# Optimization experiments

Hardware: AMD Instinct MI355X
Metric: run time of the kernel (lower is better)

Reference implementation:

```python
import jax, jax.numpy as jnp
import numpy as np
from jax import lax

D_MODEL = 1024
D_INNER = 2048   # expand=2.0
D_CONV = 4
D_STATE = 16     # delta=16
DT_RANK = 64     # ceil(d_model/16)
B, L = 4, 2048


def setup_inputs() -> dict:
    key = jax.random.key(0)
    ks = jax.random.split(key, 8)
    x = jax.random.normal(ks[0], (B, L, D_MODEL), jnp.float32)
    W_in = jax.random.normal(ks[1], (2 * D_INNER, D_MODEL), jnp.float32) * 0.02
    conv_w = jax.random.normal(ks[2], (D_INNER, D_CONV), jnp.float32) * 0.2
    conv_b = jnp.zeros((D_INNER,), jnp.float32)
    W_x = jax.random.normal(ks[3], (DT_RANK + 2 * D_STATE, D_INNER), jnp.float32) * 0.02
    W_dt = jax.random.normal(ks[4], (D_INNER, DT_RANK), jnp.float32) * 0.1
    # bias so softplus(b_dt) ~ dt in [1e-3, 1e-1] as in mamba_ssm init
    b_dt = jax.random.normal(ks[5], (D_INNER,), jnp.float32) * 0.3 - 4.0
    # mamba S4D-real init: A = -(1..d_state)
    A_log = jnp.log(jnp.tile(jnp.arange(1, D_STATE + 1, dtype=jnp.float32), (D_INNER, 1)))
    D_skip = jnp.ones((D_INNER,), jnp.float32)
    W_out = jax.random.normal(ks[6], (D_MODEL, D_INNER), jnp.float32) * 0.02
    return {"x": x, "W_in": W_in, "conv_w": conv_w, "conv_b": conv_b,
            "W_x": W_x, "W_dt": W_dt, "b_dt": b_dt, "A_log": A_log,
            "D_skip": D_skip, "W_out": W_out}


def reference(x, W_in, conv_w, conv_b, W_x, W_dt, b_dt, A_log, D_skip, W_out):
    Bsz, Lseq, _ = x.shape
    # input projection -> (B, L, 2*d_inner); split into ssm branch xi and gate z
    xz = jnp.einsum('bld,ed->ble', x, W_in)
    xi, z = jnp.split(xz, 2, axis=-1)
    # causal depthwise conv over sequence (pad left by d_conv-1), then SiLU
    xc = lax.conv_general_dilated(
        xi.transpose(0, 2, 1),               # (B, d_inner, L)
        conv_w[:, None, :],                  # (d_inner, 1, d_conv)
        window_strides=(1,),
        padding=[(D_CONV - 1, 0)],
        dimension_numbers=('NCH', 'OIH', 'NCH'),
        feature_group_count=D_INNER)
    xc = jax.nn.silu(xc + conv_b[None, :, None]).transpose(0, 2, 1)  # (B, L, d_inner)
    # data-dependent SSM params
    xdbl = jnp.einsum('bld,ed->ble', xc, W_x)          # (B, L, dt_rank + 2*d_state)
    dt_lo = xdbl[..., :DT_RANK]
    Bm = xdbl[..., DT_RANK:DT_RANK + D_STATE]          # (B, L, d_state)
    Cm = xdbl[..., DT_RANK + D_STATE:]                 # (B, L, d_state)
    dt = jax.nn.softplus(jnp.einsum('blr,dr->bld', dt_lo, W_dt) + b_dt)  # (B, L, d_inner)
    A = -jnp.exp(A_log)                                # (d_inner, d_state)

    def step(h, inp):
        dt_t, x_t, B_t, C_t = inp                      # (B,Di), (B,Di), (B,S), (B,S)
        dA = jnp.exp(dt_t[..., None] * A)              # (B, Di, S)
        h = dA * h + (dt_t * x_t)[..., None] * B_t[:, None, :]
        y = jnp.einsum('bds,bs->bd', h, C_t)
        return h, y

    h0 = jnp.zeros((Bsz, D_INNER, D_STATE), x.dtype)
    inputs = (dt.transpose(1, 0, 2), xc.transpose(1, 0, 2),
              Bm.transpose(1, 0, 2), Cm.transpose(1, 0, 2))
    _, ys = lax.scan(step, h0, inputs)                 # ys: (L, B, d_inner)
    y = ys.transpose(1, 0, 2) + xc * D_skip            # skip connection
    y = y * jax.nn.silu(z)                             # gating
    return jnp.einsum('bld,ed->ble', y, W_out)         # (B, L, d_model)
```

## Files before the change

kernel.cpp:

```cpp
#include <hip/hip_runtime.h>
#include <hip/hip_bf16.h>

#define DM    1024
#define DI    2048
#define DCONV 4
#define DSTATE 16
#define DRANK 64
#define BB    4
#define LSEQ  2048
#define MM    (BB*LSEQ)
#define CHUNK 64

typedef _Float16 f16x8 __attribute__((ext_vector_type(8)));
typedef _Float16 f16x4 __attribute__((ext_vector_type(4)));
typedef float    f32x4 __attribute__((ext_vector_type(4)));

#define SWIZ(row, g) ((((row) * 4) + ((g) ^ ((row) & 3) ^ (((row) >> 2) & 1))) * 8)

__global__ __launch_bounds__(256) void split_kernel(
    const float* __restrict__ in, _Float16* __restrict__ hi,
    _Float16* __restrict__ lo, int n4)
{
    const int i = blockIdx.x * 256 + threadIdx.x;
    if (i >= n4) return;
    const float4 v = ((const float4*)in)[i];
    _Float16 h[4], l[4];
    h[0] = (_Float16)v.x; l[0] = (_Float16)(v.x - (float)h[0]);
    h[1] = (_Float16)v.y; l[1] = (_Float16)(v.y - (float)h[1]);
    h[2] = (_Float16)v.z; l[2] = (_Float16)(v.z - (float)h[2]);
    h[3] = (_Float16)v.w; l[3] = (_Float16)(v.w - (float)h[3]);
    *(uint2*)&hi[(size_t)i * 4] = *(uint2*)h;
    *(uint2*)&lo[(size_t)i * 4] = *(uint2*)l;
}

__global__ __launch_bounds__(256) void gemm_nt_split(
    float* __restrict__ C,
    const _Float16* __restrict__ Ah, const _Float16* __restrict__ Al,
    const _Float16* __restrict__ Bh, const _Float16* __restrict__ Bl,
    int M, int N, int K)
{
    __shared__ __align__(16) _Float16 sAh[128 * 32];
    __shared__ __align__(16) _Float16 sAl[128 * 32];
    __shared__ __align__(16) _Float16 sBh[128 * 32];
    __shared__ __align__(16) _Float16 sBl[128 * 32];

    const int t = threadIdx.x;
    const int m0 = blockIdx.y * 128, n0 = blockIdx.x * 128;
    const int l = t & 63, w = t >> 6;
    const int wr = w >> 1, wc = w & 1;
    const int fr = l & 15, fg = l >> 4;

    f32x4 acc[4][4];
    const f32x4 zz = {0.f, 0.f, 0.f, 0.f};
#pragma unroll
    for (int i = 0; i < 4; ++i)
#pragma unroll
        for (int j = 0; j < 4; ++j) acc[i][j] = zz;

    const int r0 = t >> 2, c0 = t & 3;
    const int r1 = r0 + 64, c1 = c0;
    const int d0 = SWIZ(r0, c0), d1 = SWIZ(r1, c1);
    const size_t gA0 = (size_t)(m0 + r0) * K + c0 * 8;
    const size_t gA1 = (size_t)(m0 + r1) * K + c1 * 8;
    const size_t gB0 = (size_t)(n0 + r0) * K + c0 * 8;
    const size_t gB1 = (size_t)(n0 + r1) * K + c1 * 8;

    uint4 vAh0 = *(const uint4*)&Ah[gA0], vAh1 = *(const uint4*)&Ah[gA1];
    uint4 vAl0 = *(const uint4*)&Al[gA0], vAl1 = *(const uint4*)&Al[gA1];
    uint4 vBh0 = *(const uint4*)&Bh[gB0], vBh1 = *(const uint4*)&Bh[gB1];
    uint4 vBl0 = *(const uint4*)&Bl[gB0], vBl1 = *(const uint4*)&Bl[gB1];

    const int nk = K / 32;
    for (int kt = 0; kt < nk; ++kt) {
        __syncthreads();
        *(uint4*)&sAh[d0] = vAh0;  *(uint4*)&sAh[d1] = vAh1;
        *(uint4*)&sAl[d0] = vAl0;  *(uint4*)&sAl[d1] = vAl1;
        *(uint4*)&sBh[d0] = vBh0;  *(uint4*)&sBh[d1] = vBh1;
        *(uint4*)&sBl[d0] = vBl0;  *(uint4*)&sBl[d1] = vBl1;
        __syncthreads();

        if (kt + 1 < nk) {
            const size_t o = (size_t)(kt + 1) * 32;
            vAh0 = *(const uint4*)&Ah[gA0 + o]; vAh1 = *(const uint4*)&Ah[gA1 + o];
            vAl0 = *(const uint4*)&Al[gA0 + o]; vAl1 = *(const uint4*)&Al[gA1 + o];
            vBh0 = *(const uint4*)&Bh[gB0 + o]; vBh1 = *(const uint4*)&Bh[gB1 + o];
            vBl0 = *(const uint4*)&Bl[gB0 + o]; vBl1 = *(const uint4*)&Bl[gB1 + o];
        }

        f16x8 fbh[4], fbl[4];
#pragma unroll
        for (int nr = 0; nr < 4; ++nr) {
            const int row = wc * 64 + nr * 16 + fr;
            const int ad = SWIZ(row, fg);
            fbh[nr] = *(const f16x8*)&sBh[ad];
            fbl[nr] = *(const f16x8*)&sBl[ad];
        }
#pragma unroll
        for (int mr = 0; mr < 4; ++mr) {
            const int row = wr * 64 + mr * 16 + fr;
            const int ad = SWIZ(row, fg);
            const f16x8 fah = *(const f16x8*)&sAh[ad];
            const f16x8 fal = *(const f16x8*)&sAl[ad];
#pragma unroll
            for (int nr = 0; nr < 4; ++nr) {
                acc[mr][nr] = __builtin_amdgcn_mfma_f32_16x16x32_f16(
                    fah, fbh[nr], acc[mr][nr], 0, 0, 0);
                acc[mr][nr] = __builtin_amdgcn_mfma_f32_16x16x32_f16(
                    fah, fbl[nr], acc[mr][nr], 0, 0, 0);
                acc[mr][nr] = __builtin_amdgcn_mfma_f32_16x16x32_f16(
                    fal, fbh[nr], acc[mr][nr], 0, 0, 0);
            }
        }
    }

#pragma unroll
    for (int mr = 0; mr < 4; ++mr)
#pragma unroll
        for (int nr = 0; nr < 4; ++nr) {
            const int col = n0 + wc * 64 + nr * 16 + fr;
#pragma unroll
            for (int q = 0; q < 4; ++q) {
                const int rowc = m0 + wr * 64 + mr * 16 + fg * 4 + q;
                C[(size_t)rowc * N + col] = acc[mr][nr][q];
            }
        }
}

__global__ __launch_bounds__(256) void conv_silu_split_kernel(
    const float* __restrict__ xi, const float* __restrict__ cw,
    const float* __restrict__ cb, _Float16* __restrict__ xch,
    _Float16* __restrict__ xcl)
{
    const int idx = blockIdx.x * 256 + threadIdx.x;
    const int d4 = idx & (DI / 4 - 1);
    const int bl = idx / (DI / 4);
    const int l  = bl & (LSEQ - 1);
    const int d  = d4 * 4;

    float4 acc = *(const float4*)&cb[d];
    const float4 w0 = *(const float4*)&cw[(d + 0) * 4];
    const float4 w1 = *(const float4*)&cw[(d + 1) * 4];
    const float4 w2 = *(const float4*)&cw[(d + 2) * 4];
    const float4 w3 = *(const float4*)&cw[(d + 3) * 4];

#pragma unroll
    for (int k = 0; k < 4; ++k) {
        const int ll = l - 3 + k;
        if (ll < 0) continue;
        const float4 xv = *(const float4*)&xi[(size_t)(bl - 3 + k) * DI + d];
        const float wk0 = (k == 0) ? w0.x : (k == 1) ? w0.y : (k == 2) ? w0.z : w0.w;
        const float wk1 = (k == 0) ? w1.x : (k == 1) ? w1.y : (k == 2) ? w1.z : w1.w;
        const float wk2 = (k == 0) ? w2.x : (k == 1) ? w2.y : (k == 2) ? w2.z : w2.w;
        const float wk3 = (k == 0) ? w3.x : (k == 1) ? w3.y : (k == 2) ? w3.z : w3.w;
        acc.x = fmaf(xv.x, wk0, acc.x);
        acc.y = fmaf(xv.y, wk1, acc.y);
        acc.z = fmaf(xv.z, wk2, acc.z);
        acc.w = fmaf(xv.w, wk3, acc.w);
    }
    acc.x = acc.x / (1.f + __expf(-acc.x));
    acc.y = acc.y / (1.f + __expf(-acc.y));
    acc.z = acc.z / (1.f + __expf(-acc.z));
    acc.w = acc.w / (1.f + __expf(-acc.w));

    _Float16 h[4], lo4[4];
    h[0] = (_Float16)acc.x; lo4[0] = (_Float16)(acc.x - (float)h[0]);
    h[1] = (_Float16)acc.y; lo4[1] = (_Float16)(acc.y - (float)h[1]);
    h[2] = (_Float16)acc.z; lo4[2] = (_Float16)(acc.z - (float)h[2]);
    h[3] = (_Float16)acc.w; lo4[3] = (_Float16)(acc.w - (float)h[3]);
    *(uint2*)&xch[(size_t)bl * DI + d] = *(uint2*)h;
    *(uint2*)&xcl[(size_t)bl * DI + d] = *(uint2*)lo4;
}

__global__ __launch_bounds__(256) void xdbl_mfma_kernel(
    const _Float16* __restrict__ Xh, const _Float16* __restrict__ Xl,
    const _Float16* __restrict__ Wh, const _Float16* __restrict__ Wl,
    float* __restrict__ xdbl)
{
    __shared__ __align__(16) _Float16 sXh[64 * 32];
    __shared__ __align__(16) _Float16 sXl[64 * 32];
    __shared__ __align__(16) _Float16 sWh[96 * 32];
    __shared__ __align__(16) _Float16 sWl[96 * 32];

    const int t = threadIdx.x;
    const int m0 = blockIdx.x * 64;
    const int l = t & 63, w = t >> 6;
    const int fr = l & 15, fg = l >> 4;

    f32x4 acc[6];
    const f32x4 zz = {0.f, 0.f, 0.f, 0.f};
#pragma unroll
    for (int i = 0; i < 6; ++i) acc[i] = zz;

    const int ar = t >> 2, ac = t & 3;
    const int da = SWIZ(ar, ac);
    const size_t gX = (size_t)(m0 + ar) * DI + ac * 8;
    const int br0 = t >> 2, bc0 = t & 3;
    const int db0 = SWIZ(br0, bc0);
    const size_t gW0 = (size_t)br0 * DI + bc0 * 8;
    const bool has1 = t < 128;
    const int br1 = (t + 256) >> 2, bc1 = t & 3;
    const int db1 = SWIZ(br1, bc1);
    const size_t gW1 = (size_t)br1 * DI + bc1 * 8;

    uint4 vXh = *(const uint4*)&Xh[gX], vXl = *(const uint4*)&Xl[gX];
    uint4 vWh0 = *(const uint4*)&Wh[gW0], vWl0 = *(const uint4*)&Wl[gW0];
    uint4 vWh1, vWl1;
    if (has1) { vWh1 = *(const uint4*)&Wh[gW1]; vWl1 = *(const uint4*)&Wl[gW1]; }

    const int nk = DI / 32;
    for (int kt = 0; kt < nk; ++kt) {
        __syncthreads();
        *(uint4*)&sXh[da] = vXh;   *(uint4*)&sXl[da] = vXl;
        *(uint4*)&sWh[db0] = vWh0; *(uint4*)&sWl[db0] = vWl0;
        if (has1) { *(uint4*)&sWh[db1] = vWh1; *(uint4*)&sWl[db1] = vWl1; }
        __syncthreads();

        if (kt + 1 < nk) {
            const size_t o = (size_t)(kt + 1) * 32;
            vXh = *(const uint4*)&Xh[gX + o];   vXl = *(const uint4*)&Xl[gX + o];
            vWh0 = *(const uint4*)&Wh[gW0 + o]; vWl0 = *(const uint4*)&Wl[gW0 + o];
            if (has1) { vWh1 = *(const uint4*)&Wh[gW1 + o]; vWl1 = *(const uint4*)&Wl[gW1 + o]; }
        }

        const int aad = SWIZ(w * 16 + fr, fg);
        const f16x8 fah = *(const f16x8*)&sXh[aad];
        const f16x8 fal = *(const f16x8*)&sXl[aad];
#pragma unroll
        for (int nr = 0; nr < 6; ++nr) {
            const int bad = SWIZ(nr * 16 + fr, fg);
            const f16x8 fbh = *(const f16x8*)&sWh[bad];
            const f16x8 fbl = *(const f16x8*)&sWl[bad];
            acc[nr] = __builtin_amdgcn_mfma_f32_16x16x32_f16(fah, fbh, acc[nr], 0, 0, 0);
            acc[nr] = __builtin_amdgcn_mfma_f32_16x16x32_f16(fah, fbl, acc[nr], 0, 0, 0);
            acc[nr] = __builtin_amdgcn_mfma_f32_16x16x32_f16(fal, fbh, acc[nr], 0, 0, 0);
        }
    }

#pragma unroll
    for (int nr = 0; nr < 6; ++nr) {
        const int col = nr * 16 + fr;
#pragma unroll
        for (int q = 0; q < 4; ++q) {
            const int row = m0 + w * 16 + fg * 4 + q;
            xdbl[(size_t)row * 96 + col] = acc[nr][q];
        }
    }
}

__global__ __launch_bounds__(256) void dt_kernel(
    const float* __restrict__ xdbl, const float* __restrict__ Wdt,
    const float* __restrict__ bdt, float* __restrict__ dt)
{
    __shared__ float s[16][64];
    const int t = threadIdx.x;
    const int m0 = blockIdx.y * 16;

    {
        const int row = t >> 4, c4 = t & 15;
        *(float4*)&s[row][c4 * 4] =
            *(const float4*)&xdbl[(size_t)(m0 + row) * 96 + c4 * 4];
    }
    __syncthreads();

    const int n = blockIdx.x * 256 + t;
    float4 w[16];
#pragma unroll
    for (int k4 = 0; k4 < 16; ++k4)
        w[k4] = *(const float4*)&Wdt[(size_t)n * 64 + k4 * 4];
    const float bd = bdt[n];

#pragma unroll
    for (int i = 0; i < 16; ++i) {
        float acc = bd;
#pragma unroll
        for (int k4 = 0; k4 < 16; ++k4) {
            acc += s[i][k4*4+0] * w[k4].x + s[i][k4*4+1] * w[k4].y
                 + s[i][k4*4+2] * w[k4].z + s[i][k4*4+3] * w[k4].w;
        }
        const float sp = (acc > 20.f) ? acc : log1pf(__expf(acc));
        dt[(size_t)(m0 + i) * DI + n] = sp;
    }
}

__global__ __launch_bounds__(256) void scan_kernel(
    const float* __restrict__ dt,
    const _Float16* __restrict__ xch, const _Float16* __restrict__ xcl,
    const float* __restrict__ xdbl, const float* z,
    const float* __restrict__ A_log, const float* __restrict__ D_skip,
    float* y)
{
    __shared__ float s_dt[CHUNK][16];
    __shared__ float s_xc[CHUNK][16];
    __shared__ float s_z [CHUNK][16];
    __shared__ float s_B [CHUNK][16];
    __shared__ float s_C [CHUNK][16];
    __shared__ float s_p [16][16][17];
    __shared__ float s_D [16];

    const int t = threadIdx.x;
    const int g = t >> 4;
    const int s = t & 15;
    const int c = blockIdx.x * 16 + g;
    const int b = c >> 11;
    const int d = c & (DI - 1);
    const int d0 = (blockIdx.x * 16) & (DI - 1);

    const int lr = t >> 2;
    const int lc = t & 3;

    if (t < 16) s_D[t] = D_skip[d0 + t];

    const float Acoef = -__expf(A_log[d * DSTATE + s]);
    const size_t rbase = (size_t)b * LSEQ;

    float h = 0.f;
    float4 r_dt, r_z, r_B, r_C;
    f16x4 r_xh, r_xl;

    {
        const size_t row = rbase + lr;
        r_dt = *(const float4*)&dt[row * DI + d0 + lc * 4];
        r_xh = *(const f16x4*)&xch[row * DI + d0 + lc * 4];
        r_xl = *(const f16x4*)&xcl[row * DI + d0 + lc * 4];
        r_z  = *(const float4*)&z [row * DI + d0 + lc * 4];
        r_B  = *(const float4*)&xdbl[row * 96 + DRANK + lc * 4];
        r_C  = *(const float4*)&xdbl[row * 96 + DRANK + DSTATE + lc * 4];
    }

    for (int ch = 0; ch < LSEQ / CHUNK; ++ch) {
        __syncthreads();
        *(float4*)&s_dt[lr][lc * 4] = r_dt;
        {
            float4 xf;
            xf.x = (float)r_xh[0] + (float)r_xl[0];
            xf.y = (float)r_xh[1] + (float)r_xl[1];
            xf.z = (float)r_xh[2] + (float)r_xl[2];
            xf.w = (float)r_xh[3] + (float)r_xl[3];
            *(float4*)&s_xc[lr][lc * 4] = xf;
        }
        *(float4*)&s_z [lr][lc * 4] = r_z;
        *(float4*)&s_B [lr][lc * 4] = r_B;
        *(float4*)&s_C [lr][lc * 4] = r_C;
        __syncthreads();

        if (ch + 1 < LSEQ / CHUNK) {
            const size_t row = rbase + (size_t)(ch + 1) * CHUNK + lr;
            r_dt = *(const float4*)&dt[row * DI + d0 + lc * 4];
            r_xh = *(const f16x4*)&xch[row * DI + d0 + lc * 4];
            r_xl = *(const f16x4*)&xcl[row * DI + d0 + lc * 4];
            r_z  = *(const float4*)&z [row * DI + d0 + lc * 4];
            r_B  = *(const float4*)&xdbl[row * 96 + DRANK + lc * 4];
            r_C  = *(const float4*)&xdbl[row * 96 + DRANK + DSTATE + lc * 4];
        }

#pragma unroll
        for (int sub = 0; sub < CHUNK / 16; ++sub) {
            const int base = sub * 16;
            float dA[16], u[16], Cv[16];
#pragma unroll
            for (int j = 0; j < 16; ++j) {
                const float dtv = s_dt[base + j][g];
                const float xv  = s_xc[base + j][g];
                const float Bv  = s_B [base + j][s];
                Cv[j] = s_C[base + j][s];
                dA[j] = __expf(dtv * Acoef);
                u[j]  = dtv * xv * Bv;
            }
#pragma unroll
            for (int j = 0; j < 16; ++j) {
                h = fmaf(dA[j], h, u[j]);
                s_p[g][j][s] = h * Cv[j];
            }
            __syncthreads();
            float accp = 0.f;
#pragma unroll
            for (int k = 0; k < 16; ++k)
                accp += s_p[g][s][k];
            {
                const int row = base + s;
                const float xv = s_xc[row][g];
                const float zv = s_z [row][g];
                const float sig = 1.f / (1.f + __expf(-zv));
                s_z[row][g] = fmaf(xv, s_D[g], accp) * (zv * sig);
            }
            __syncthreads();
        }
        {
            const size_t row = rbase + (size_t)ch * CHUNK + lr;
            *(float4*)&y[row * DI + d0 + lc * 4] = *(const float4*)&s_z[lr][lc * 4];
        }
    }
}

extern "C" void kernel_launch(void* const* d_in, const int* in_sizes, int n_in,
                              void* d_out, int out_size, void* d_ws, size_t ws_size,
                              hipStream_t stream)
{
    const float* x      = (const float*)d_in[0];
    const float* W_in   = (const float*)d_in[1];
    const float* cw     = (const float*)d_in[2];
    const float* cb     = (const float*)d_in[3];
    const float* W_x    = (const float*)d_in[4];
    const float* W_dt   = (const float*)d_in[5];
    const float* b_dt   = (const float*)d_in[6];
    const float* A_log  = (const float*)d_in[7];
    const float* D_skip = (const float*)d_in[8];
    const float* W_out  = (const float*)d_in[9];
    float* out = (float*)d_out;

    const size_t MMDI = (size_t)MM * DI;
    float* xi  = (float*)d_ws;
    float* zb  = xi  + MMDI;
    float* xcb = zb  + MMDI;
    float* xdb = xcb + MMDI;

    _Float16* xh   = (_Float16*)xcb;
    _Float16* xl   = xh + (size_t)MM * DM;
    _Float16* Winh = xl + (size_t)MM * DM;
    _Float16* Winl = Winh + (size_t)2 * DI * DM;
    _Float16* xch  = (_Float16*)xcb;
    _Float16* xcl  = xch + MMDI;
    _Float16* Wxh  = (_Float16*)xi;
    _Float16* Wxl  = Wxh + (size_t)96 * DI;
    _Float16* yh   = (_Float16*)xcb;
    _Float16* yl   = yh + MMDI;
    _Float16* Woh  = (_Float16*)xi;
    _Float16* Wol  = Woh + (size_t)DM * DI;

    const dim3 blk(256);

    split_kernel<<<dim3((MM * DM / 4) / 256), blk, 0, stream>>>(x, xh, xl, MM * DM / 4);
    split_kernel<<<dim3((2 * DI * DM / 4) / 256), blk, 0, stream>>>(
        W_in, Winh, Winl, 2 * DI * DM / 4);

    gemm_nt_split<<<dim3(DI / 128, MM / 128), blk, 0, stream>>>(
        xi, xh, xl, Winh, Winl, MM, DI, DM);
    gemm_nt_split<<<dim3(DI / 128, MM / 128), blk, 0, stream>>>(
        zb, xh, xl, Winh + (size_t)DI * DM, Winl + (size_t)DI * DM, MM, DI, DM);

    conv_silu_split_kernel<<<dim3(MM * (DI / 4) / 256), blk, 0, stream>>>(
        xi, cw, cb, xch, xcl);

    split_kernel<<<dim3((96 * DI / 4) / 256), blk, 0, stream>>>(
        W_x, Wxh, Wxl, 96 * DI / 4);

    xdbl_mfma_kernel<<<dim3(MM / 64), blk, 0, stream>>>(xch, xcl, Wxh, Wxl, xdb);

    dt_kernel<<<dim3(DI / 256, MM / 16), blk, 0, stream>>>(xdb, W_dt, b_dt, xi);

    scan_kernel<<<dim3(BB * DI / 16), blk, 0, stream>>>(
        xi, xch, xcl, xdb, zb, A_log, D_skip, zb);

    split_kernel<<<dim3((MM * DI / 4) / 256), blk, 0, stream>>>(zb, yh, yl, MM * DI / 4);
    split_kernel<<<dim3((DM * DI / 4) / 256), blk, 0, stream>>>(
        W_out, Woh, Wol, DM * DI / 4);

    gemm_nt_split<<<dim3(DM / 128, MM / 128), blk, 0, stream>>>(
        out, yh, yl, Woh, Wol, MM, DM, DI);
}
```

Measured before the change: 827.3 us.

## Use direct global-to-LDS loads in split GEMM and MFMA for dt projection

Result: faster. 788.9 us (-4.6%).

```diff
diff --git a/kernel.cpp b/kernel.cpp
--- a/kernel.cpp
+++ b/kernel.cpp
@@ -15,7 +15,12 @@
 typedef _Float16 f16x4 __attribute__((ext_vector_type(4)));
 typedef float    f32x4 __attribute__((ext_vector_type(4)));
 
-#define SWIZ(row, g) ((((row) * 4) + ((g) ^ ((row) & 3) ^ (((row) >> 2) & 1))) * 8)
+#define SWIZMASK(row) (((row) & 3) ^ (((row) >> 2) & 1))
+#define SWIZ(row, g)  ((((row) * 4) + ((g) ^ SWIZMASK(row))) * 8)
+
+#define GLOAD_LDS16(gp, sp) __builtin_amdgcn_global_load_lds( \
+    (const __attribute__((address_space(1))) void*)(gp),      \
+    (__attribute__((address_space(3))) void*)(sp), 16, 0, 0)
 
 __global__ __launch_bounds__(256) void split_kernel(
     const float* __restrict__ in, _Float16* __restrict__ hi,
@@ -57,35 +62,28 @@
 #pragma unroll
         for (int j = 0; j < 4; ++j) acc[i][j] = zz;
 
-    const int r0 = t >> 2, c0 = t & 3;
-    const int r1 = r0 + 64, c1 = c0;
-    const int d0 = SWIZ(r0, c0), d1 = SWIZ(r1, c1);
-    const size_t gA0 = (size_t)(m0 + r0) * K + c0 * 8;
-    const size_t gA1 = (size_t)(m0 + r1) * K + c1 * 8;
-    const size_t gB0 = (size_t)(n0 + r0) * K + c0 * 8;
-    const size_t gB1 = (size_t)(n0 + r1) * K + c1 * 8;
-
-    uint4 vAh0 = *(const uint4*)&Ah[gA0], vAh1 = *(const uint4*)&Ah[gA1];
-    uint4 vAl0 = *(const uint4*)&Al[gA0], vAl1 = *(const uint4*)&Al[gA1];
-    uint4 vBh0 = *(const uint4*)&Bh[gB0], vBh1 = *(const uint4*)&Bh[gB1];
-    uint4 vBl0 = *(const uint4*)&Bl[gB0], vBl1 = *(const uint4*)&Bl[gB1];
+    const int ch0 = w * 2, ch1 = w * 2 + 1;
+    const int g4 = l & 3;
+    const int rA0 = ch0 * 16 + (l >> 2), rA1 = ch1 * 16 + (l >> 2);
+    const int c0 = (g4 ^ SWIZMASK(rA0)) * 8, c1 = (g4 ^ SWIZMASK(rA1)) * 8;
+    const size_t gA0 = (size_t)(m0 + rA0) * K + c0;
+    const size_t gA1 = (size_t)(m0 + rA1) * K + c1;
+    const size_t gB0 = (size_t)(n0 + rA0) * K + c0;
+    const size_t gB1 = (size_t)(n0 + rA1) * K + c1;
+    const int lo0 = ch0 * 512, lo1 = ch1 * 512;
 
     const int nk = K / 32;
     for (int kt = 0; kt < nk; ++kt) {
-        __syncthreads();
-        *(uint4*)&sAh[d0] = vAh0;  *(uint4*)&sAh[d1] = vAh1;
-        *(uint4*)&sAl[d0] = vAl0;  *(uint4*)&sAl[d1] = vAl1;
-        *(uint4*)&sBh[d0] = vBh0;  *(uint4*)&sBh[d1] = vBh1;
-        *(uint4*)&sBl[d0] = vBl0;  *(uint4*)&sBl[d1] = vBl1;
-        __syncthreads();
-
-        if (kt + 1 < nk) {
-            const size_t o = (size_t)(kt + 1) * 32;
-            vAh0 = *(const uint4*)&Ah[gA0 + o]; vAh1 = *(const uint4*)&Ah[gA1 + o];
-            vAl0 = *(const uint4*)&Al[gA0 + o]; vAl1 = *(const uint4*)&Al[gA1 + o];
-            vBh0 = *(const uint4*)&Bh[gB0 + o]; vBh1 = *(const uint4*)&Bh[gB1 + o];
-            vBl0 = *(const uint4*)&Bl[gB0 + o]; vBl1 = *(const uint4*)&Bl[gB1 + o];
-        }
+        const size_t ko = (size_t)kt * 32;
+        GLOAD_LDS16(&Ah[gA0 + ko], &sAh[lo0]);
+        GLOAD_LDS16(&Ah[gA1 + ko], &sAh[lo1]);
+        GLOAD_LDS16(&Al[gA0 + ko], &sAl[lo0]);
+        GLOAD_LDS16(&Al[gA1 + ko], &sAl[lo1]);
+        GLOAD_LDS16(&Bh[gB0 + ko], &sBh[lo0]);
+        GLOAD_LDS16(&Bh[gB1 + ko], &sBh[lo1]);
+        GLOAD_LDS16(&Bl[gB0 + ko], &sBl[lo0]);
+        GLOAD_LDS16(&Bl[gB1 + ko], &sBl[lo1]);
+        __syncthreads();
 
         f16x8 fbh[4], fbl[4];
 #pragma unroll
@@ -111,6 +109,7 @@
                     fal, fbh[nr], acc[mr][nr], 0, 0, 0);
             }
         }
+        __syncthreads();
     }
 
 #pragma unroll
@@ -122,6 +121,105 @@
             for (int q = 0; q < 4; ++q) {
                 const int rowc = m0 + wr * 64 + mr * 16 + fg * 4 + q;
                 C[(size_t)rowc * N + col] = acc[mr][nr][q];
+            }
+        }
+}
+
+__global__ __launch_bounds__(256) void dt_mfma_kernel(
+    const float* __restrict__ xdbl, const float* __restrict__ Wdt,
+    const float* __restrict__ bdt, float* __restrict__ dtout)
+{
+    __shared__ __align__(16) _Float16 sAh[128 * 32];
+    __shared__ __align__(16) _Float16 sAl[128 * 32];
+    __shared__ __align__(16) _Float16 sBh[128 * 32];
+    __shared__ __align__(16) _Float16 sBl[128 * 32];
+
+    const int t = threadIdx.x;
+    const int m0 = blockIdx.y * 128, n0 = blockIdx.x * 128;
+    const int l = t & 63, w = t >> 6;
+    const int wr = w >> 1, wc = w & 1;
+    const int fr = l & 15, fg = l >> 4;
+
+    f32x4 acc[4][4];
+    const f32x4 zz = {0.f, 0.f, 0.f, 0.f};
+#pragma unroll
+    for (int i = 0; i < 4; ++i)
+#pragma unroll
+        for (int j = 0; j < 4; ++j) acc[i][j] = zz;
+
+#pragma unroll
+    for (int kt = 0; kt < 2; ++kt) {
+        __syncthreads();
+#pragma unroll
+        for (int ss = 0; ss < 2; ++ss) {
+            const int s = t + ss * 256;
+            const int row = s >> 2, c = s & 3;
+            const int dst = SWIZ(row, c);
+            {
+                const float* p = &xdbl[(size_t)(m0 + row) * 96 + kt * 32 + c * 8];
+                const float4 a0 = *(const float4*)p, a1 = *(const float4*)(p + 4);
+                _Float16 h[8], lo8[8];
+                const float vv[8] = {a0.x,a0.y,a0.z,a0.w,a1.x,a1.y,a1.z,a1.w};
+#pragma unroll
+                for (int q = 0; q < 8; ++q) {
+                    h[q] = (_Float16)vv[q]; lo8[q] = (_Float16)(vv[q] - (float)h[q]);
+                }
+                *(uint4*)&sAh[dst] = *(uint4*)h;
+                *(uint4*)&sAl[dst] = *(uint4*)lo8;
+            }
+            {
+                const float* p = &Wdt[(size_t)(n0 + row) * 64 + kt * 32 + c * 8];
+                const float4 b0 = *(const float4*)p, b1 = *(const float4*)(p + 4);
+                _Float16 h[8], lo8[8];
+                const float vv[8] = {b0.x,b0.y,b0.z,b0.w,b1.x,b1.y,b1.z,b1.w};
+#pragma unroll
+                for (int q = 0; q < 8; ++q) {
+                    h[q] = (_Float16)vv[q]; lo8[q] = (_Float16)(vv[q] - (float)h[q]);
+                }
+                *(uint4*)&sBh[dst] = *(uint4*)h;
+                *(uint4*)&sBl[dst] = *(uint4*)lo8;
+            }
+        }
+        __syncthreads();
+
+        f16x8 fbh[4], fbl[4];
+#pragma unroll
+        for (int nr = 0; nr < 4; ++nr) {
+            const int row = wc * 64 + nr * 16 + fr;
+            const int ad = SWIZ(row, fg);
+            fbh[nr] = *(const f16x8*)&sBh[ad];
+            fbl[nr] = *(const f16x8*)&sBl[ad];
+        }
+#pragma unroll
+        for (int mr = 0; mr < 4; ++mr) {
+            const int row = wr * 64 + mr * 16 + fr;
+            const int ad = SWIZ(row, fg);
+            const f16x8 fah = *(const f16x8*)&sAh[ad];
+            const f16x8 fal = *(const f16x8*)&sAl[ad];
+#pragma unroll
+            for (int nr = 0; nr < 4; ++nr) {
+                acc[mr][nr] = __builtin_amdgcn_mfma_f32_16x16x32_f16(
+                    fah, fbh[nr], acc[mr][nr], 0, 0, 0);
+                acc[mr][nr] = __builtin_amdgcn_mfma_f32_16x16x32_f16(
+                    fah, fbl[nr], acc[mr][nr], 0, 0, 0);
+                acc[mr][nr] = __builtin_amdgcn_mfma_f32_16x16x32_f16(
+                    fal, fbh[nr], acc[mr][nr], 0, 0, 0);
+            }
+        }
+    }
+
+#pragma unroll
+    for (int mr = 0; mr < 4; ++mr)
+#pragma unroll
+        for (int nr = 0; nr < 4; ++nr) {
+            const int col = n0 + wc * 64 + nr * 16 + fr;
+            const float bd = bdt[col];
+#pragma unroll
+            for (int q = 0; q < 4; ++q) {
+                const int rowc = m0 + wr * 64 + mr * 16 + fg * 4 + q;
+                const float v = acc[mr][nr][q] + bd;
+                dtout[(size_t)rowc * DI + col] =
+                    (v > 20.f) ? v : log1pf(__expf(v));
             }
         }
 }
@@ -247,41 +345,6 @@
     }
 }
 
-__global__ __launch_bounds__(256) void dt_kernel(
-    const float* __restrict__ xdbl, const float* __restrict__ Wdt,
-    const float* __restrict__ bdt, float* __restrict__ dt)
-{
-    __shared__ float s[16][64];
-    const int t = threadIdx.x;
-    const int m0 = blockIdx.y * 16;
-
-    {
-        const int row = t >> 4, c4 = t & 15;
-        *(float4*)&s[row][c4 * 4] =
-            *(const float4*)&xdbl[(size_t)(m0 + row) * 96 + c4 * 4];
-    }
-    __syncthreads();
-
-    const int n = blockIdx.x * 256 + t;
-    float4 w[16];
-#pragma unroll
-    for (int k4 = 0; k4 < 16; ++k4)
-        w[k4] = *(const float4*)&Wdt[(size_t)n * 64 + k4 * 4];
-    const float bd = bdt[n];
-
-#pragma unroll
-    for (int i = 0; i < 16; ++i) {
-        float acc = bd;
-#pragma unroll
-        for (int k4 = 0; k4 < 16; ++k4) {
-            acc += s[i][k4*4+0] * w[k4].x + s[i][k4*4+1] * w[k4].y
-                 + s[i][k4*4+2] * w[k4].z + s[i][k4*4+3] * w[k4].w;
-        }
-        const float sp = (acc > 20.f) ? acc : log1pf(__expf(acc));
-        dt[(size_t)(m0 + i) * DI + n] = sp;
-    }
-}
-
 __global__ __launch_bounds__(256) void scan_kernel(
     const float* __restrict__ dt,
     const _Float16* __restrict__ xch, const _Float16* __restrict__ xcl,
@@ -290,8 +353,8 @@
     float* y)
 {
     __shared__ float s_dt[CHUNK][16];
-    __shared__ float s_xc[CHUNK][16];
-    __shared__ float s_z [CHUNK][16];
+    __shared__ float s_xc[CHUNK][20];
+    __shared__ float s_z [CHUNK][20];
     __shared__ float s_B [CHUNK][16];
     __shared__ float s_C [CHUNK][16];
     __shared__ float s_p [16][16][17];
@@ -446,7 +509,8 @@
 
     xdbl_mfma_kernel<<<dim3(MM / 64), blk, 0, stream>>>(xch, xcl, Wxh, Wxl, xdb);
 
-    dt_kernel<<<dim3(DI / 256, MM / 16), blk, 0, stream>>>(xdb, W_dt, b_dt, xi);
+    dt_mfma_kernel<<<dim3(DI / 128, MM / 128), blk, 0, stream>>>(
+        xdb, W_dt, b_dt, xi);
 
     scan_kernel<<<dim3(BB * DI / 16), blk, 0, stream>>>(
         xi, xch, xcl, xdb, zb, A_log, D_skip, zb);
```
